# Kernel optimization log

Hardware: AMD Instinct MI355X
Metric: run time of the kernel (lower is better)

## Reference

```python
import jax, jax.numpy as jnp
import numpy as np

N_NODES = 100000
N_EDGES = 1600000
IN_CH = 128
HIDDEN = 64
N_CLASSES = 40


def setup_inputs() -> dict:
    key = jax.random.key(0)
    k_x, k_e, k_w1, k_w2 = jax.random.split(key, 4)
    x = jax.random.normal(k_x, (N_NODES, IN_CH), dtype=jnp.float32)
    edge_index = jax.random.randint(k_e, (2, N_EDGES), 0, N_NODES, dtype=jnp.int64)
    # Glorot-style init for GCN weights
    W1 = jax.random.normal(k_w1, (IN_CH, HIDDEN), dtype=jnp.float32) * (1.0 / np.sqrt(IN_CH))
    b1 = jnp.zeros((HIDDEN,), dtype=jnp.float32)
    W2 = jax.random.normal(k_w2, (HIDDEN, N_CLASSES), dtype=jnp.float32) * (1.0 / np.sqrt(HIDDEN))
    b2 = jnp.zeros((N_CLASSES,), dtype=jnp.float32)
    return {"x": x, "edge_index": edge_index, "W1": W1, "b1": b1, "W2": W2, "b2": b2}


def reference(x, edge_index, W1, b1, W2, b2):
    n = x.shape[0]
    # PyG GCNConv: add self-loops, symmetric degree normalization
    loop = jnp.arange(n, dtype=edge_index.dtype)
    src = jnp.concatenate([edge_index[0], loop])  # message sources j
    dst = jnp.concatenate([edge_index[1], loop])  # aggregation targets i
    w = jnp.ones(src.shape[0], dtype=x.dtype)     # edge_weight=None -> ones
    deg = jax.ops.segment_sum(w, dst, num_segments=n)
    dinv = jnp.where(deg > 0, jax.lax.rsqrt(jnp.maximum(deg, 1e-12)), 0.0)
    norm = dinv[src] * dinv[dst]                  # [E+N]

    def gcn_conv(h, W, b):
        hw = h @ W                                # transform first (fewer flops)
        msg = hw[src] * norm[:, None]             # gather + normalize
        return jax.ops.segment_sum(msg, dst, num_segments=n) + b  # scatter-add

    h = jax.nn.relu(gcn_conv(x, W1, b1))
    # dropout is identity in eval mode
    out = gcn_conv(h, W2, b2)
    return out
```

## Files before the change

kernel.cpp:

```cpp
#include <hip/hip_runtime.h>
#include <hip/hip_bf16.h>

#define NNODES 100000
#define NEDGES 1600000
#define IN_CH 128
#define HID 64
#define NC 40
#define NPAD 100352
#define NBUK 196
#define CAP 9216
#define BCHUNK 4096
#define NBIN 391

typedef unsigned short ushort_t;
typedef unsigned int uint_t;
typedef __attribute__((ext_vector_type(8))) short short8;
typedef __attribute__((ext_vector_type(4))) float floatx4;

__device__ __forceinline__ float bf2f(ushort_t u) {
    union { unsigned int i; float f; } t;
    t.i = ((unsigned int)u) << 16;
    return t.f;
}
__device__ __forceinline__ ushort_t f2bf(float f) {
    union { float ff; unsigned int i; } t;
    t.ff = f;
    unsigned int r = t.i + 0x7fff + ((t.i >> 16) & 1);
    return (ushort_t)(r >> 16);
}
__device__ __forceinline__ float2 unpk(uint_t p) {
    union { unsigned int i; float f; } a, b;
    a.i = p << 16;
    b.i = p & 0xffff0000u;
    return make_float2(a.f, b.f);
}

__global__ void k_ginit(int* __restrict__ gcur) {
    int b = threadIdx.x;
    if (b < NBUK) gcur[b] = b * CAP;
}

__global__ __launch_bounds__(256) void k_bin0(
    const int* __restrict__ srcs, const int* __restrict__ dsts,
    int* __restrict__ gcur, uint_t* __restrict__ tmp, int e)
{
    __shared__ uint_t pk[BCHUNK];
    __shared__ ushort_t bk[BCHUNK];
    __shared__ int hist[NBUK];
    __shared__ int base[NBUK];
    int t = threadIdx.x;
    int begin = blockIdx.x * BCHUNK;
    int cnt = e - begin; if (cnt > BCHUNK) cnt = BCHUNK;

    for (int i = t; i < NBUK; i += 256) hist[i] = 0;
    __syncthreads();
    for (int j = t; j < cnt; j += 256) {
        int d = dsts[begin + j];
        int s = srcs[begin + j];
        int b = d >> 9;
        pk[j] = (uint_t)s | ((uint_t)(d & 511) << 17);
        bk[j] = (ushort_t)b;
        atomicAdd(&hist[b], 1);
    }
    __syncthreads();
    for (int i = t; i < NBUK; i += 256) {
        base[i] = atomicAdd(&gcur[i], hist[i]);
        hist[i] = 0;
    }
    __syncthreads();
    for (int j = t; j < cnt; j += 256) {
        int b = bk[j];
        int r = atomicAdd(&hist[b], 1);
        int pos = base[b] + r;
        if (pos < (b + 1) * CAP) tmp[pos] = pk[j];
    }
}

__global__ __launch_bounds__(256) void k_bbase(const int* __restrict__ gcur,
                                               int* __restrict__ bbase, int e) {
    __shared__ int s[256];
    int t = threadIdx.x;
    int c = (t < NBUK) ? (gcur[t] - t * CAP) : 0;
    s[t] = c;
    __syncthreads();
    for (int off = 1; off < 256; off <<= 1) {
        int v = (t >= off) ? s[t - off] : 0;
        __syncthreads();
        s[t] += v;
        __syncthreads();
    }
    if (t < NBUK) bbase[t] = s[t] - c;
    if (t == 0) bbase[NBUK] = e;
}

__global__ __launch_bounds__(256) void k_sort_a(
    const uint_t* __restrict__ tmp, const int* __restrict__ gcur,
    const int* __restrict__ bbase, int* __restrict__ row_start,
    float* __restrict__ dinv, int n, int e)
{
    __shared__ int cnt[512];
    __shared__ int sc[512];
    int t = threadIdx.x;
    int b = blockIdx.x;
    int d0 = b << 9;
    int total = gcur[b] - b * CAP;
    cnt[t] = 0; cnt[t + 256] = 0;
    __syncthreads();
    const uint_t* seg = tmp + b * CAP;
    for (int j = t; j < total; j += 256)
        atomicAdd(&cnt[seg[j] >> 17], 1);
    __syncthreads();
    sc[t] = cnt[t]; sc[t + 256] = cnt[t + 256];
    __syncthreads();
    for (int off = 1; off < 512; off <<= 1) {
        int v0 = (t >= off) ? sc[t - off] : 0;
        int i1 = t + 256;
        int v1 = (i1 >= off) ? sc[i1 - off] : 0;
        __syncthreads();
        sc[t] += v0; sc[i1] += v1;
        __syncthreads();
    }
    int gb = bbase[b];
#pragma unroll
    for (int q = 0; q < 2; ++q) {
        int i = t + q * 256;
        int node = d0 + i;
        if (node < n) {
            row_start[node] = gb + sc[i] - cnt[i];
            dinv[node] = rsqrtf((float)cnt[i] + 1.0f);
        }
    }
    if (b == NBUK - 1 && t == 0) row_start[n] = e;
}

__global__ __launch_bounds__(256) void k_sort_b(
    const uint_t* __restrict__ tmp, const int* __restrict__ gcur,
    const int* __restrict__ row_start, uint_t* __restrict__ es, int n)
{
    __shared__ int cur[512];
    int t = threadIdx.x;
    int b = blockIdx.x;
    int d0 = b << 9;
    int total = gcur[b] - b * CAP;
#pragma unroll
    for (int q = 0; q < 2; ++q) {
        int i = t + q * 256;
        int node = d0 + i;
        cur[i] = (node < n) ? row_start[node] : 0;
    }
    __syncthreads();
    const uint_t* seg = tmp + b * CAP;
    for (int j = t; j < total; j += 256) {
        uint_t p = seg[j];
        int ld = (int)(p >> 17);
        int pos = atomicAdd(&cur[ld], 1);
        es[pos] = p & 0x1FFFFu;
    }
}

__global__ void k_prepw(const float* __restrict__ W1, ushort_t* __restrict__ Wp) {
    int i = blockIdx.x * 256 + threadIdx.x;
    if (i >= IN_CH * HID) return;
    int j = i & 7;
    int m = (i >> 3) & 15;
    int ct = (i >> 7) & 3;
    int quad = (i >> 9) & 3;
    int kc = i >> 11;
    int k = kc * 32 + quad * 8 + j;
    int c = ct * 16 + m;
    Wp[i] = f2bf(W1[k * HID + c]);
}

__global__ __launch_bounds__(256) void k_gemm1(
    const float* __restrict__ x, const ushort_t* __restrict__ Wp,
    const float* __restrict__ dinv, ushort_t* __restrict__ hw1, int n)
{
    int wave = threadIdx.x >> 6;
    int lane = threadIdx.x & 63;
    int m = lane & 15;
    int quad = lane >> 4;
    int row = blockIdx.x * 64 + wave * 16 + m;
    int rowc = row < n ? row : (n - 1);
    const float* xr = x + (size_t)rowc * IN_CH + quad * 8;

    floatx4 acc[4];
#pragma unroll
    for (int ct = 0; ct < 4; ++ct) acc[ct] = (floatx4){0.f, 0.f, 0.f, 0.f};

#pragma unroll
    for (int kc = 0; kc < 4; ++kc) {
        float4 xa = *(const float4*)(xr + kc * 32);
        float4 xb = *(const float4*)(xr + kc * 32 + 4);
        short8 a;
        a[0] = (short)f2bf(xa.x); a[1] = (short)f2bf(xa.y);
        a[2] = (short)f2bf(xa.z); a[3] = (short)f2bf(xa.w);
        a[4] = (short)f2bf(xb.x); a[5] = (short)f2bf(xb.y);
        a[6] = (short)f2bf(xb.z); a[7] = (short)f2bf(xb.w);
#pragma unroll
        for (int ct = 0; ct < 4; ++ct) {
            short8 b = *(const short8*)(Wp + ((((kc * 4 + quad) * 4 + ct) * 16 + m) << 3));
            acc[ct] = __builtin_amdgcn_mfma_f32_16x16x32_bf16(a, b, acc[ct], 0, 0, 0);
        }
    }
    int r0 = blockIdx.x * 64 + wave * 16 + quad * 4;
#pragma unroll
    for (int r = 0; r < 4; ++r) {
        int rr = r0 + r;
        if (rr < n) {
            float di = dinv[rr];
            ushort_t* o = hw1 + (size_t)rr * HID + m;
#pragma unroll
            for (int ct = 0; ct < 4; ++ct) o[ct * 16] = f2bf(acc[ct][r] * di);
        } else if (rr == n) {
            ushort_t* o = hw1 + (size_t)n * HID + m;
#pragma unroll
            for (int ct = 0; ct < 4; ++ct) o[ct * 16] = 0;
        }
    }
}

__global__ __launch_bounds__(256) void k_agg1(
    const int* __restrict__ row_start, const uint_t* __restrict__ es,
    const float* __restrict__ dinv, const uint_t* __restrict__ hw1u,
    const float* __restrict__ b1, float* __restrict__ h, int n)
{
    int lane = threadIdx.x & 63;
    int qbase = lane & 48;
    int ll = lane & 15;
    int node = blockIdx.x * 16 + (threadIdx.x >> 4);
    bool valid = node < n;
    int rs = valid ? row_start[node] : 0;
    int re = valid ? row_start[node + 1] : 0;
    float di = valid ? dinv[node] : 0.f;
    int selfrow = valid ? node : n;

    float a0, a1, a2, a3;
    {
        uint2 p = *(const uint2*)(hw1u + (size_t)selfrow * 32 + ll * 2);
        float2 v0 = unpk(p.x), v1 = unpk(p.y);
        a0 = v0.x; a1 = v0.y; a2 = v1.x; a3 = v1.y;
    }
    for (int base = rs; base < re; base += 16) {
        int idx = base + ll;
        int el = (idx < re) ? (int)es[idx] : n;
        int nw = re - base;
        uint2 pA[8], pB[8];
#pragma unroll
        for (int b = 0; b < 8; ++b) {
            int s = __shfl(el, qbase + b);
            pA[b] = *(const uint2*)(hw1u + (size_t)s * 32 + ll * 2);
        }
        bool more = nw > 8;
        if (more) {
#pragma unroll
            for (int b = 0; b < 8; ++b) {
                int s = __shfl(el, qbase + 8 + b);
                pB[b] = *(const uint2*)(hw1u + (size_t)s * 32 + ll * 2);
            }
        }
#pragma unroll
        for (int b = 0; b < 8; ++b) {
            float2 v0 = unpk(pA[b].x), v1 = unpk(pA[b].y);
            a0 += v0.x; a1 += v0.y; a2 += v1.x; a3 += v1.y;
        }
        if (more) {
#pragma unroll
            for (int b = 0; b < 8; ++b) {
                float2 v0 = unpk(pB[b].x), v1 = unpk(pB[b].y);
                a0 += v0.x; a1 += v0.y; a2 += v1.x; a3 += v1.y;
            }
        }
    }
    if (valid) {
        float4 bb = ((const float4*)b1)[ll];
        float4 o;
        o.x = fmaxf(a0 * di + bb.x, 0.f);
        o.y = fmaxf(a1 * di + bb.y, 0.f);
        o.z = fmaxf(a2 * di + bb.z, 0.f);
        o.w = fmaxf(a3 * di + bb.w, 0.f);
        ((float4*)(h + (size_t)node * 64))[ll] = o;
    }
}

__global__ __launch_bounds__(256) void k_gemm2(
    const float* __restrict__ h, const float* __restrict__ W2,
    const float* __restrict__ dinv, ushort_t* __restrict__ hw2, int n)
{
    __shared__ float wsm[HID * NC];
    for (int i = threadIdx.x; i < HID * NC; i += 256) wsm[i] = W2[i];
    __syncthreads();
    int row = blockIdx.x * 256 + threadIdx.x;
    if (row > n) return;
    unsigned int* o = (unsigned int*)(hw2 + (size_t)row * NC);
    if (row == n) {
#pragma unroll
        for (int c2 = 0; c2 < NC / 2; ++c2) o[c2] = 0;
        return;
    }
    const float4* hr = (const float4*)(h + (size_t)row * HID);
    float acc[NC];
#pragma unroll
    for (int c = 0; c < NC; ++c) acc[c] = 0.f;
#pragma unroll 4
    for (int k4 = 0; k4 < HID / 4; ++k4) {
        float4 hv = hr[k4];
        const float* w0 = wsm + (k4 * 4) * NC;
#pragma unroll
        for (int c = 0; c < NC; ++c)
            acc[c] += hv.x * w0[c] + hv.y * w0[c + NC] + hv.z * w0[c + 2 * NC] + hv.w * w0[c + 3 * NC];
    }
    float di = dinv[row];
#pragma unroll
    for (int c2 = 0; c2 < NC / 2; ++c2)
        o[c2] = (unsigned int)f2bf(acc[2 * c2] * di) | ((unsigned int)f2bf(acc[2 * c2 + 1] * di) << 16);
}

__global__ __launch_bounds__(256) void k_agg2(
    const int* __restrict__ row_start, const uint_t* __restrict__ es,
    const float* __restrict__ dinv, const uint_t* __restrict__ hw2u,
    const float* __restrict__ b2, float* __restrict__ out, int n)
{
    int lane = threadIdx.x & 63;
    int qbase = lane & 48;
    int ll = lane & 15;
    int lc = (ll < 10) ? ll : 0;
    int node = blockIdx.x * 16 + (threadIdx.x >> 4);
    bool valid = node < n;
    int rs = valid ? row_start[node] : 0;
    int re = valid ? row_start[node + 1] : 0;
    float di = valid ? dinv[node] : 0.f;
    int selfrow = valid ? node : n;

    float a0, a1, a2, a3;
    {
        uint2 p = *(const uint2*)(hw2u + (size_t)selfrow * 20 + lc * 2);
        float2 v0 = unpk(p.x), v1 = unpk(p.y);
        a0 = v0.x; a1 = v0.y; a2 = v1.x; a3 = v1.y;
    }
    for (int base = rs; base < re; base += 16) {
        int idx = base + ll;
        int el = (idx < re) ? (int)es[idx] : n;
        int nw = re - base;
        uint2 pA[8], pB[8];
#pragma unroll
        for (int b = 0; b < 8; ++b) {
            int s = __shfl(el, qbase + b);
            pA[b] = *(const uint2*)(hw2u + (size_t)s * 20 + lc * 2);
        }
        bool more = nw > 8;
        if (more) {
#pragma unroll
            for (int b = 0; b < 8; ++b) {
                int s = __shfl(el, qbase + 8 + b);
                pB[b] = *(const uint2*)(hw2u + (size_t)s * 20 + lc * 2);
            }
        }
#pragma unroll
        for (int b = 0; b < 8; ++b) {
            float2 v0 = unpk(pA[b].x), v1 = unpk(pA[b].y);
            a0 += v0.x; a1 += v0.y; a2 += v1.x; a3 += v1.y;
        }
        if (more) {
#pragma unroll
            for (int b = 0; b < 8; ++b) {
                float2 v0 = unpk(pB[b].x), v1 = unpk(pB[b].y);
                a0 += v0.x; a1 += v0.y; a2 += v1.x; a3 += v1.y;
            }
        }
    }
    if (valid && ll < 10) {
        float4 bb = ((const float4*)b2)[ll];
        float4 o;
        o.x = a0 * di + bb.x;
        o.y = a1 * di + bb.y;
        o.z = a2 * di + bb.z;
        o.w = a3 * di + bb.w;
        ((float4*)(out + (size_t)node * 40))[ll] = o;
    }
}

extern "C" void kernel_launch(void* const* d_in, const int* in_sizes, int n_in,
                              void* d_out, int out_size, void* d_ws, size_t ws_size,
                              hipStream_t stream) {
    const float* x  = (const float*)d_in[0];
    const int* edge = (const int*)d_in[1];
    const float* W1 = (const float*)d_in[2];
    const float* b1 = (const float*)d_in[3];
    const float* W2 = (const float*)d_in[4];
    const float* b2 = (const float*)d_in[5];
    float* out      = (float*)d_out;

    const int n = in_sizes[0] / IN_CH;
    const int e = in_sizes[1] / 2;
    const int* srcs = edge;
    const int* dsts = edge + e;

    int*      gcur      = (int*)d_ws;
    int*      bbase     = gcur + 256;
    int*      row_start = bbase + 256;
    float*    dinv      = (float*)(row_start + NPAD);
    uint_t*   tmp       = (uint_t*)(dinv + NPAD);
    uint_t*   es        = tmp + (size_t)NBUK * CAP;
    ushort_t* Wp        = (ushort_t*)(es + NEDGES);
    ushort_t* hw1       = Wp + 8192;
    float*    h         = (float*)(hw1 + (size_t)(NNODES + 1) * HID);
    ushort_t* hw2       = (ushort_t*)(h + (size_t)NNODES * HID);

    k_ginit<<<1, 256, 0, stream>>>(gcur);
    k_bin0<<<NBIN, 256, 0, stream>>>(srcs, dsts, gcur, tmp, e);
    k_bbase<<<1, 256, 0, stream>>>(gcur, bbase, e);
    k_sort_a<<<NBUK, 256, 0, stream>>>(tmp, gcur, bbase, row_start, dinv, n, e);
    k_sort_b<<<NBUK, 256, 0, stream>>>(tmp, gcur, row_start, es, n);

    k_prepw<<<32, 256, 0, stream>>>(W1, Wp);
    k_gemm1<<<(n + 63) / 64, 256, 0, stream>>>(x, Wp, dinv, hw1, n);
    k_agg1<<<(n + 15) / 16, 256, 0, stream>>>(row_start, es, dinv, (const uint_t*)hw1, b1, h, n);
    k_gemm2<<<(n + 255) / 256, 256, 0, stream>>>(h, W2, dinv, hw2, n);
    k_agg2<<<(n + 15) / 16, 256, 0, stream>>>(row_start, es, dinv, (const uint_t*)hw2, b2, out, n);
}
```

Measured before the change: 248.6 us.

## Fuse GEMM2 into layer-1 aggregation and merge sort/init kernels

```diff
diff --git a/kernel.cpp b/kernel.cpp
--- a/kernel.cpp
+++ b/kernel.cpp
@@ -11,6 +11,7 @@
 #define CAP 9216
 #define BCHUNK 4096
 #define NBIN 391
+#define HW2S 64
 
 typedef unsigned short ushort_t;
 typedef unsigned int uint_t;
@@ -35,9 +36,25 @@
     return make_float2(a.f, b.f);
 }
 
-__global__ void k_ginit(int* __restrict__ gcur) {
-    int b = threadIdx.x;
-    if (b < NBUK) gcur[b] = b * CAP;
+__global__ __launch_bounds__(256) void k_init(
+    const float* __restrict__ W1, ushort_t* __restrict__ Wp,
+    int* __restrict__ gcur, ushort_t* __restrict__ hw2, int n)
+{
+    int b = blockIdx.x, t = threadIdx.x;
+    if (b < 32) {
+        int i = b * 256 + t;
+        int j = i & 7;
+        int m = (i >> 3) & 15;
+        int ct = (i >> 7) & 3;
+        int quad = (i >> 9) & 3;
+        int kc = i >> 11;
+        int k = kc * 32 + quad * 8 + j;
+        int c = ct * 16 + m;
+        Wp[i] = f2bf(W1[k * HID + c]);
+    } else {
+        if (t < NBUK) gcur[t] = t * CAP;
+        if (t >= 224 && t < 224 + NC) hw2[(size_t)n * HW2S + (t - 224)] = 0;
+    }
 }
 
 __global__ __launch_bounds__(256) void k_bin0(
@@ -76,36 +93,29 @@
     }
 }
 
-__global__ __launch_bounds__(256) void k_bbase(const int* __restrict__ gcur,
-                                               int* __restrict__ bbase, int e) {
-    __shared__ int s[256];
-    int t = threadIdx.x;
-    int c = (t < NBUK) ? (gcur[t] - t * CAP) : 0;
-    s[t] = c;
-    __syncthreads();
-    for (int off = 1; off < 256; off <<= 1) {
-        int v = (t >= off) ? s[t - off] : 0;
-        __syncthreads();
-        s[t] += v;
-        __syncthreads();
-    }
-    if (t < NBUK) bbase[t] = s[t] - c;
-    if (t == 0) bbase[NBUK] = e;
-}
-
-__global__ __launch_bounds__(256) void k_sort_a(
+__global__ __launch_bounds__(256) void k_sort(
     const uint_t* __restrict__ tmp, const int* __restrict__ gcur,
-    const int* __restrict__ bbase, int* __restrict__ row_start,
-    float* __restrict__ dinv, int n, int e)
+    int* __restrict__ row_start, float* __restrict__ dinv,
+    uint_t* __restrict__ es, int n, int e)
 {
     __shared__ int cnt[512];
     __shared__ int sc[512];
+    __shared__ int red[256];
     int t = threadIdx.x;
     int b = blockIdx.x;
     int d0 = b << 9;
     int total = gcur[b] - b * CAP;
+    if (total > CAP) total = CAP;
+    int part = 0;
+    for (int i = t; i < b; i += 256) part += gcur[i] - i * CAP;
+    red[t] = part;
     cnt[t] = 0; cnt[t + 256] = 0;
     __syncthreads();
+    for (int off = 128; off > 0; off >>= 1) {
+        if (t < off) red[t] += red[t + off];
+        __syncthreads();
+    }
+    int gb = red[0];
     const uint_t* seg = tmp + b * CAP;
     for (int j = t; j < total; j += 256)
         atomicAdd(&cnt[seg[j] >> 17], 1);
@@ -120,55 +130,25 @@
         sc[t] += v0; sc[i1] += v1;
         __syncthreads();
     }
-    int gb = bbase[b];
 #pragma unroll
     for (int q = 0; q < 2; ++q) {
         int i = t + q * 256;
         int node = d0 + i;
+        int start = gb + sc[i] - cnt[i];
         if (node < n) {
-            row_start[node] = gb + sc[i] - cnt[i];
+            row_start[node] = start;
             dinv[node] = rsqrtf((float)cnt[i] + 1.0f);
         }
-    }
-    if (b == NBUK - 1 && t == 0) row_start[n] = e;
-}
-
-__global__ __launch_bounds__(256) void k_sort_b(
-    const uint_t* __restrict__ tmp, const int* __restrict__ gcur,
-    const int* __restrict__ row_start, uint_t* __restrict__ es, int n)
-{
-    __shared__ int cur[512];
-    int t = threadIdx.x;
-    int b = blockIdx.x;
-    int d0 = b << 9;
-    int total = gcur[b] - b * CAP;
-#pragma unroll
-    for (int q = 0; q < 2; ++q) {
-        int i = t + q * 256;
-        int node = d0 + i;
-        cur[i] = (node < n) ? row_start[node] : 0;
-    }
-    __syncthreads();
-    const uint_t* seg = tmp + b * CAP;
+        cnt[i] = start;
+    }
+    __syncthreads();
     for (int j = t; j < total; j += 256) {
         uint_t p = seg[j];
         int ld = (int)(p >> 17);
-        int pos = atomicAdd(&cur[ld], 1);
+        int pos = atomicAdd(&cnt[ld], 1);
         es[pos] = p & 0x1FFFFu;
     }
-}
-
-__global__ void k_prepw(const float* __restrict__ W1, ushort_t* __restrict__ Wp) {
-    int i = blockIdx.x * 256 + threadIdx.x;
-    if (i >= IN_CH * HID) return;
-    int j = i & 7;
-    int m = (i >> 3) & 15;
-    int ct = (i >> 7) & 3;
-    int quad = (i >> 9) & 3;
-    int kc = i >> 11;
-    int k = kc * 32 + quad * 8 + j;
-    int c = ct * 16 + m;
-    Wp[i] = f2bf(W1[k * HID + c]);
+    if (b == NBUK - 1 && t == 0) row_start[n] = e;
 }
 
 __global__ __launch_bounds__(256) void k_gemm1(
@@ -222,12 +202,19 @@
 __global__ __launch_bounds__(256) void k_agg1(
     const int* __restrict__ row_start, const uint_t* __restrict__ es,
     const float* __restrict__ dinv, const uint_t* __restrict__ hw1u,
-    const float* __restrict__ b1, float* __restrict__ h, int n)
-{
+    const float* __restrict__ b1, const float* __restrict__ W2,
+    ushort_t* __restrict__ hw2, int n)
+{
+    __shared__ float wsm[HID * NC];
+    __shared__ float hsm[16][68];
+    for (int i = threadIdx.x; i < HID * NC; i += 256) wsm[i] = W2[i];
+    __syncthreads();
+
     int lane = threadIdx.x & 63;
     int qbase = lane & 48;
     int ll = lane & 15;
-    int node = blockIdx.x * 16 + (threadIdx.x >> 4);
+    int q16 = threadIdx.x >> 4;
+    int node = blockIdx.x * 16 + q16;
     bool valid = node < n;
     int rs = valid ? row_start[node] : 0;
     int re = valid ? row_start[node + 1] : 0;
@@ -271,48 +258,36 @@
             }
         }
     }
-    if (valid) {
+    float4 hv;
+    {
         float4 bb = ((const float4*)b1)[ll];
-        float4 o;
-        o.x = fmaxf(a0 * di + bb.x, 0.f);
-        o.y = fmaxf(a1 * di + bb.y, 0.f);
-        o.z = fmaxf(a2 * di + bb.z, 0.f);
-        o.w = fmaxf(a3 * di + bb.w, 0.f);
-        ((float4*)(h + (size_t)node * 64))[ll] = o;
-    }
-}
-
-__global__ __launch_bounds__(256) void k_gemm2(
-    const float* __restrict__ h, const float* __restrict__ W2,
-    const float* __restrict__ dinv, ushort_t* __restrict__ hw2, int n)
-{
-    __shared__ float wsm[HID * NC];
-    for (int i = threadIdx.x; i < HID * NC; i += 256) wsm[i] = W2[i];
-    __syncthreads();
-    int row = blockIdx.x * 256 + threadIdx.x;
-    if (row > n) return;
-    unsigned int* o = (unsigned int*)(hw2 + (size_t)row * NC);
-    if (row == n) {
-#pragma unroll
-        for (int c2 = 0; c2 < NC / 2; ++c2) o[c2] = 0;
-        return;
-    }
-    const float4* hr = (const float4*)(h + (size_t)row * HID);
-    float acc[NC];
-#pragma unroll
-    for (int c = 0; c < NC; ++c) acc[c] = 0.f;
+        hv.x = fmaxf(a0 * di + bb.x, 0.f);
+        hv.y = fmaxf(a1 * di + bb.y, 0.f);
+        hv.z = fmaxf(a2 * di + bb.z, 0.f);
+        hv.w = fmaxf(a3 * di + bb.w, 0.f);
+    }
+    *(float4*)&hsm[q16][ll * 4] = hv;
+    int lw = (ll < 10) ? ll : 0;
+    const float4* w4 = (const float4*)wsm;
+    float4 acc = make_float4(0.f, 0.f, 0.f, 0.f);
 #pragma unroll 4
-    for (int k4 = 0; k4 < HID / 4; ++k4) {
-        float4 hv = hr[k4];
-        const float* w0 = wsm + (k4 * 4) * NC;
-#pragma unroll
-        for (int c = 0; c < NC; ++c)
-            acc[c] += hv.x * w0[c] + hv.y * w0[c + NC] + hv.z * w0[c + 2 * NC] + hv.w * w0[c + 3 * NC];
-    }
-    float di = dinv[row];
-#pragma unroll
-    for (int c2 = 0; c2 < NC / 2; ++c2)
-        o[c2] = (unsigned int)f2bf(acc[2 * c2] * di) | ((unsigned int)f2bf(acc[2 * c2 + 1] * di) << 16);
+    for (int k4 = 0; k4 < 16; ++k4) {
+        float4 hk = *(const float4*)&hsm[q16][k4 * 4];
+        float4 w0 = w4[(k4 * 4 + 0) * 10 + lw];
+        float4 w1 = w4[(k4 * 4 + 1) * 10 + lw];
+        float4 w2 = w4[(k4 * 4 + 2) * 10 + lw];
+        float4 w3 = w4[(k4 * 4 + 3) * 10 + lw];
+        acc.x += hk.x * w0.x + hk.y * w1.x + hk.z * w2.x + hk.w * w3.x;
+        acc.y += hk.x * w0.y + hk.y * w1.y + hk.z * w2.y + hk.w * w3.y;
+        acc.z += hk.x * w0.z + hk.y * w1.z + hk.z * w2.z + hk.w * w3.z;
+        acc.w += hk.x * w0.w + hk.y * w1.w + hk.z * w2.w + hk.w * w3.w;
+    }
+    if (valid && ll < 10) {
+        uint2 st;
+        st.x = (uint_t)f2bf(acc.x * di) | ((uint_t)f2bf(acc.y * di) << 16);
+        st.y = (uint_t)f2bf(acc.z * di) | ((uint_t)f2bf(acc.w * di) << 16);
+        *(uint2*)(hw2 + (size_t)node * HW2S + ll * 4) = st;
+    }
 }
 
 __global__ __launch_bounds__(256) void k_agg2(
@@ -333,7 +308,7 @@
 
     float a0, a1, a2, a3;
     {
-        uint2 p = *(const uint2*)(hw2u + (size_t)selfrow * 20 + lc * 2);
+        uint2 p = *(const uint2*)(hw2u + (size_t)selfrow * (HW2S / 2) + lc * 2);
         float2 v0 = unpk(p.x), v1 = unpk(p.y);
         a0 = v0.x; a1 = v0.y; a2 = v1.x; a3 = v1.y;
     }
@@ -345,14 +320,14 @@
 #pragma unroll
         for (int b = 0; b < 8; ++b) {
             int s = __shfl(el, qbase + b);
-            pA[b] = *(const uint2*)(hw2u + (size_t)s * 20 + lc * 2);
+            pA[b] = *(const uint2*)(hw2u + (size_t)s * (HW2S / 2) + lc * 2);
         }
         bool more = nw > 8;
         if (more) {
 #pragma unroll
             for (int b = 0; b < 8; ++b) {
                 int s = __shfl(el, qbase + 8 + b);
-                pB[b] = *(const uint2*)(hw2u + (size_t)s * 20 + lc * 2);
+                pB[b] = *(const uint2*)(hw2u + (size_t)s * (HW2S / 2) + lc * 2);
             }
         }
 #pragma unroll
@@ -396,25 +371,18 @@
     const int* dsts = edge + e;
 
     int*      gcur      = (int*)d_ws;
-    int*      bbase     = gcur + 256;
-    int*      row_start = bbase + 256;
+    int*      row_start = gcur + 256;
     float*    dinv      = (float*)(row_start + NPAD);
     uint_t*   tmp       = (uint_t*)(dinv + NPAD);
     uint_t*   es        = tmp + (size_t)NBUK * CAP;
     ushort_t* Wp        = (ushort_t*)(es + NEDGES);
     ushort_t* hw1       = Wp + 8192;
-    float*    h         = (float*)(hw1 + (size_t)(NNODES + 1) * HID);
-    ushort_t* hw2       = (ushort_t*)(h + (size_t)NNODES * HID);
-
-    k_ginit<<<1, 256, 0, stream>>>(gcur);
+    ushort_t* hw2       = hw1 + (size_t)(NNODES + 1) * HID;
+
+    k_init<<<33, 256, 0, stream>>>(W1, Wp, gcur, hw2, n);
     k_bin0<<<NBIN, 256, 0, stream>>>(srcs, dsts, gcur, tmp, e);
-    k_bbase<<<1, 256, 0, stream>>>(gcur, bbase, e);
-    k_sort_a<<<NBUK, 256, 0, stream>>>(tmp, gcur, bbase, row_start, dinv, n, e);
-    k_sort_b<<<NBUK, 256, 0, stream>>>(tmp, gcur, row_start, es, n);
-
-    k_prepw<<<32, 256, 0, stream>>>(W1, Wp);
+    k_sort<<<NBUK, 256, 0, stream>>>(tmp, gcur, row_start, dinv, es, n, e);
     k_gemm1<<<(n + 63) / 64, 256, 0, stream>>>(x, Wp, dinv, hw1, n);
-    k_agg1<<<(n + 15) / 16, 256, 0, stream>>>(row_start, es, dinv, (const uint_t*)hw1, b1, h, n);
-    k_gemm2<<<(n + 255) / 256, 256, 0, stream>>>(h, W2, dinv, hw2, n);
+    k_agg1<<<(n + 15) / 16, 256, 0, stream>>>(row_start, es, dinv, (const uint_t*)hw1, b1, W2, hw2, n);
     k_agg2<<<(n + 15) / 16, 256, 0, stream>>>(row_start, es, dinv, (const uint_t*)hw2, b2, out, n);
 }
```

After: 228.1 us. 1.09x faster.
